# Performance work log

Hardware: AMD Instinct MI355X
Metric: run time of the kernel (lower is better)

The kernel has to match this reference:

```python
import jax, jax.numpy as jnp
import numpy as np


def axisangle2mat(p):
    # p: [N, 6] = (rotation vector rx,ry,rz, translation tx,ty,tz) -> [N, 3, 4]
    v = p[:, :3]
    t = p[:, 3:]
    theta = jnp.sqrt(jnp.sum(v * v, axis=-1) + 1e-12)  # [N]
    k = v / theta[:, None]
    kx, ky, kz = k[:, 0], k[:, 1], k[:, 2]
    zero = jnp.zeros_like(kx)
    K = jnp.stack([
        jnp.stack([zero, -kz, ky], -1),
        jnp.stack([kz, zero, -kx], -1),
        jnp.stack([-ky, kx, zero], -1),
    ], -2)  # [N,3,3]
    I = jnp.eye(3, dtype=p.dtype)
    s = jnp.sin(theta)[:, None, None]
    c = (1.0 - jnp.cos(theta))[:, None, None]
    R = I + s * K + c * jnp.matmul(K, K)
    return jnp.concatenate([R, t[:, :, None]], axis=-1)  # [N,3,4]


def grid_sample_3d(vol, grid):
    # vol: [D,H,W]; grid: [...,3] with last dim (x,y,z) in [-1,1].
    # Replicates F.grid_sample(mode='bilinear', padding_mode='zeros', align_corners=False).
    D, H, W = vol.shape
    ix = ((grid[..., 0] + 1.0) * W - 1.0) * 0.5
    iy = ((grid[..., 1] + 1.0) * H - 1.0) * 0.5
    iz = ((grid[..., 2] + 1.0) * D - 1.0) * 0.5
    x0 = jnp.floor(ix); y0 = jnp.floor(iy); z0 = jnp.floor(iz)
    fx = ix - x0; fy = iy - y0; fz = iz - z0
    vol_flat = vol.reshape(-1)
    out = jnp.zeros(grid.shape[:-1], vol.dtype)
    for dz in (0, 1):
        for dy in (0, 1):
            for dx in (0, 1):
                xc = x0 + dx; yc = y0 + dy; zc = z0 + dz
                wgt = ((fx if dx else 1.0 - fx) * (fy if dy else 1.0 - fy) * (fz if dz else 1.0 - fz))
                valid = ((xc >= 0) & (xc < W) & (yc >= 0) & (yc < H) & (zc >= 0) & (zc < D))
                xi = jnp.clip(xc, 0, W - 1).astype(jnp.int32)
                yi = jnp.clip(yc, 0, H - 1).astype(jnp.int32)
                zi = jnp.clip(zc, 0, D - 1).astype(jnp.int32)
                v = vol_flat[(zi * H + yi) * W + xi]
                out = out + jnp.where(valid, v * wgt, 0.0)
    return out


def setup_inputs() -> dict:
    key = jax.random.key(0)
    ks = jax.random.split(key, 8)
    B, n, D, H, W = 4096, 2048, 256, 256, 256
    x = jax.random.normal(ks[0], (1, 1, D, H, W), dtype=jnp.float32)
    # voxel-space sample points inside the volume
    sampleGrid = jax.random.uniform(ks[1], (B, 3), dtype=jnp.float32) * jnp.array([W - 1, H - 1, D - 1], jnp.float32)
    ax = jnp.concatenate([
        jax.random.normal(ks[2], (B, 1, 3), dtype=jnp.float32) * 0.1,   # small rotations
        jax.random.normal(ks[3], (B, 1, 3), dtype=jnp.float32) * 5.0,   # translations (voxels)
    ], axis=-1)
    low = jax.random.uniform(ks[4], (B, 1, 3), dtype=jnp.float32) * 2.0
    ext = jax.random.uniform(ks[5], (B, 1, 3), dtype=jnp.float32) * 4.0 + 1.0
    bound = jnp.concatenate([low, low + ext], axis=1)  # [B,2,3], bound[:,1] > bound[:,0]
    A = jax.random.normal(ks[6], (B, 3, 3), dtype=jnp.float32) * 0.3
    InvCovScaled = jnp.einsum('bij,bkj->bik', A, A) + 0.5 * jnp.eye(3, dtype=jnp.float32)  # SPD
    xyz_psf = jax.random.normal(ks[7], (B, n, 3), dtype=jnp.float32)
    psf_sigma = jnp.ones((1,), jnp.float32)  # unused in forward (as in the original)
    return dict(x=x, sampleGrid=sampleGrid, ax=ax, bound=bound,
                InvCovScaled=InvCovScaled, psf_sigma=psf_sigma, xyz_psf=xyz_psf)


def reference(x, sampleGrid, ax, bound, InvCovScaled, psf_sigma, xyz_psf):
    # x: [1,1,D,H,W]; sampleGrid: [B,3]; ax: [B,1,6]; bound: [B,2,3];
    # InvCovScaled: [B,3,3]; xyz_psf: [B,n,3] (the torch.randn draw, made explicit)
    W = x.shape[-1]; H = x.shape[-2]; D = x.shape[-3]
    size = (W, H, D)  # matches torch: size = [x.shape[-1], x.shape[-2], x.shape[-3]]
    scaled_xyz_psf = 2.0 * jax.nn.sigmoid(xyz_psf) - 1.0                      # [B,n,3]
    half = (bound[:, 1, :] - bound[:, 0, :]) * 0.5                            # [B,3]
    bound_psf = scaled_xyz_psf * half[:, None]                                # [B,n,3]
    mat = axisangle2mat(ax.reshape(-1, 6)).reshape(ax.shape[:-1] + (3, 4))    # [B,1,3,4]
    R = mat[:, 0, :, :3]                                                      # [B,3,3]
    T = mat[:, 0, :, 3]                                                       # [B,3]
    # trans_first=True: R @ (p + T)
    mat_sampleGrid = jnp.einsum('bij,bj->bi', R, sampleGrid + T)[:, None]     # [B,1,3]
    psf_sampleGrid = mat_sampleGrid + bound_psf                               # [B,n,3]
    norm = jnp.array([size[0] - 1, size[1] - 1, size[2] - 1], psf_sampleGrid.dtype)
    grid = 2.0 * (psf_sampleGrid / norm - 0.5)
    psf_x = grid_sample_3d(x[0, 0], grid)                                     # [B,n]
    # Mahalanobis-style weights: exp(-0.5 * c^T InvCov c)
    q = jnp.einsum('bni,bij,bnj->bn', bound_psf, InvCovScaled, bound_psf)
    w = jnp.exp(-0.5 * q)                                                     # [B,n]
    y = jnp.sum(psf_x * w, axis=-1) / jnp.sum(w, axis=-1)                     # [B]
    return y
```

## Files before the change

kernel.cpp:

```cpp
#include <hip/hip_runtime.h>
#include <math.h>

constexpr int NT   = 256;
constexpr int DIMV = 256;
constexpr int RS   = 8;
constexpr int RROW = 9;
constexpr int RSLICE = RS * RROW;

__global__ __launch_bounds__(NT) void psf_sample_kernel(
    const float* __restrict__ vol,
    const float* __restrict__ sampleGrid,
    const float* __restrict__ ax,
    const float* __restrict__ bound,
    const float* __restrict__ invcov,
    const float* __restrict__ xyz,
    float* __restrict__ out,
    int n)
{
    const int b   = blockIdx.x;
    const int tid = threadIdx.x;

    __shared__ float s_vol[RS * RSLICE];
    __shared__ float s_red[2 * (NT / 64)];

    const float v0 = ax[b*6+0], v1 = ax[b*6+1], v2 = ax[b*6+2];
    const float t0 = ax[b*6+3], t1 = ax[b*6+4], t2 = ax[b*6+5];
    const float theta = sqrtf(v0*v0 + v1*v1 + v2*v2 + 1e-12f);
    const float inv = 1.0f / theta;
    const float kx = v0*inv, ky = v1*inv, kz = v2*inv;
    const float sn = sinf(theta);
    const float cn = 1.0f - cosf(theta);
    const float R00 = 1.0f - cn*(ky*ky + kz*kz);
    const float R01 = -sn*kz + cn*kx*ky;
    const float R02 =  sn*ky + cn*kx*kz;
    const float R10 =  sn*kz + cn*kx*ky;
    const float R11 = 1.0f - cn*(kx*kx + kz*kz);
    const float R12 = -sn*kx + cn*ky*kz;
    const float R20 = -sn*ky + cn*kx*kz;
    const float R21 =  sn*kx + cn*ky*kz;
    const float R22 = 1.0f - cn*(kx*kx + ky*ky);
    const float g0 = sampleGrid[b*3+0] + t0;
    const float g1 = sampleGrid[b*3+1] + t1;
    const float g2 = sampleGrid[b*3+2] + t2;
    const float ms0 = R00*g0 + R01*g1 + R02*g2;
    const float ms1 = R10*g0 + R11*g1 + R12*g2;
    const float ms2 = R20*g0 + R21*g1 + R22*g2;
    const float h0 = (bound[b*6+3] - bound[b*6+0]) * 0.5f;
    const float h1 = (bound[b*6+4] - bound[b*6+1]) * 0.5f;
    const float h2 = (bound[b*6+5] - bound[b*6+2]) * 0.5f;
    const float M00 = invcov[b*9+0], M01 = invcov[b*9+1], M02 = invcov[b*9+2];
    const float M11 = invcov[b*9+4], M12 = invcov[b*9+5], M22 = invcov[b*9+8];

    const float B00 = -0.5f * M00 * h0 * h0;
    const float B11 = -0.5f * M11 * h1 * h1;
    const float B22 = -0.5f * M22 * h2 * h2;
    const float B01 = -M01 * h0 * h1;
    const float B02 = -M02 * h0 * h2;
    const float B12 = -M12 * h1 * h2;

    const float kk = 256.0f / 255.0f;
    const float cix = ms0 * kk - 0.5f;
    const float ciy = ms1 * kk - 0.5f;
    const float ciz = ms2 * kk - 0.5f;
    const float hx = h0 * kk, hy = h1 * kk, hz = h2 * kk;

    const int bx = (int)floorf(cix - hx - 1e-3f);
    const int by = (int)floorf(ciy - hy - 1e-3f);
    const int bz = (int)floorf(ciz - hz - 1e-3f);
    const bool fast = (hx <= 2.9f) && (hy <= 2.9f) && (hz <= 2.9f);

    if (fast) {
        #pragma unroll
        for (int pass = 0; pass < (RS*RS*RS)/NT; ++pass) {
            const int idx = pass * NT + tid;
            const int lx = idx & 7, ly = (idx >> 3) & 7, lz = idx >> 6;
            const int gx = bx + lx, gy = by + ly, gz = bz + lz;
            float v = 0.0f;
            if ((unsigned)gx < (unsigned)DIMV && (unsigned)gy < (unsigned)DIMV &&
                (unsigned)gz < (unsigned)DIMV)
                v = vol[((size_t)gz * DIMV + gy) * DIMV + gx];
            s_vol[(lz * RS + ly) * RROW + lx] = v;
        }
    }
    __syncthreads();

    float sum_wx = 0.0f, sum_w = 0.0f;

    auto doSample = [&](float rx, float ry, float rz) {
        const float ex = __expf(-rx), ey = __expf(-ry), ez = __expf(-rz);
        const float sx = (1.0f - ex) * __builtin_amdgcn_rcpf(1.0f + ex);
        const float sy = (1.0f - ey) * __builtin_amdgcn_rcpf(1.0f + ey);
        const float sz = (1.0f - ez) * __builtin_amdgcn_rcpf(1.0f + ez);

        const float ixf = fmaf(sx, hx, cix);
        const float iyf = fmaf(sy, hy, ciy);
        const float izf = fmaf(sz, hz, ciz);
        const float x0f = floorf(ixf), y0f = floorf(iyf), z0f = floorf(izf);
        const float fx = ixf - x0f, fy = iyf - y0f, fz = izf - z0f;

        float val;
        if (fast) {
            const int lx = (int)x0f - bx;
            const int ly = (int)y0f - by;
            const int lz = (int)z0f - bz;
            const float* p = &s_vol[(lz * RS + ly) * RROW + lx];
            const float v000 = p[0],              v001 = p[1];
            const float v010 = p[RROW],           v011 = p[RROW + 1];
            const float v100 = p[RSLICE],         v101 = p[RSLICE + 1];
            const float v110 = p[RSLICE + RROW],  v111 = p[RSLICE + RROW + 1];
            const float a00 = fmaf(fx, v001 - v000, v000);
            const float a01 = fmaf(fx, v011 - v010, v010);
            const float a10 = fmaf(fx, v101 - v100, v100);
            const float a11 = fmaf(fx, v111 - v110, v110);
            const float a0  = fmaf(fy, a01 - a00, a00);
            const float a1  = fmaf(fy, a11 - a10, a10);
            val = fmaf(fz, a1 - a0, a0);
        } else {
            const int x0 = (int)x0f, y0 = (int)y0f, z0 = (int)z0f;
            const int x1 = x0 + 1, y1 = y0 + 1, z1 = z0 + 1;
            const bool vx0 = (unsigned)x0 < (unsigned)DIMV;
            const bool vx1 = (unsigned)x1 < (unsigned)DIMV;
            const bool vy0 = (unsigned)y0 < (unsigned)DIMV;
            const bool vy1 = (unsigned)y1 < (unsigned)DIMV;
            const bool vz0 = (unsigned)z0 < (unsigned)DIMV;
            const bool vz1 = (unsigned)z1 < (unsigned)DIMV;
            const int cx0 = min(max(x0,0),DIMV-1), cx1 = min(max(x1,0),DIMV-1);
            const int cy0 = min(max(y0,0),DIMV-1), cy1 = min(max(y1,0),DIMV-1);
            const int cz0 = min(max(z0,0),DIMV-1), cz1 = min(max(z1,0),DIMV-1);
            const float wx0 = 1.0f-fx, wx1 = fx, wy0 = 1.0f-fy, wy1 = fy;
            const float wz0 = 1.0f-fz, wz1 = fz;
            const int r00 = (cz0*DIMV + cy0)*DIMV, r01 = (cz0*DIMV + cy1)*DIMV;
            const int r10 = (cz1*DIMV + cy0)*DIMV, r11 = (cz1*DIMV + cy1)*DIMV;
            val  = (vz0&&vy0&&vx0) ? vol[r00+cx0]*(wz0*wy0*wx0) : 0.0f;
            val += (vz0&&vy0&&vx1) ? vol[r00+cx1]*(wz0*wy0*wx1) : 0.0f;
            val += (vz0&&vy1&&vx0) ? vol[r01+cx0]*(wz0*wy1*wx0) : 0.0f;
            val += (vz0&&vy1&&vx1) ? vol[r01+cx1]*(wz0*wy1*wx1) : 0.0f;
            val += (vz1&&vy0&&vx0) ? vol[r10+cx0]*(wz1*wy0*wx0) : 0.0f;
            val += (vz1&&vy0&&vx1) ? vol[r10+cx1]*(wz1*wy0*wx1) : 0.0f;
            val += (vz1&&vy1&&vx0) ? vol[r11+cx0]*(wz1*wy1*wx0) : 0.0f;
            val += (vz1&&vy1&&vx1) ? vol[r11+cx1]*(wz1*wy1*wx1) : 0.0f;
        }

        const float f = fmaf(B00, sx*sx,
                        fmaf(B11, sy*sy,
                        fmaf(B22, sz*sz,
                        fmaf(B01, sx*sy,
                        fmaf(B02, sx*sz, B12 * (sy*sz))))));
        const float w = __expf(f);
        sum_w  += w;
        sum_wx = fmaf(w, val, sum_wx);
    };

    const int ng = n >> 2;
    const float4* __restrict__ xb4 =
        reinterpret_cast<const float4*>(xyz + (size_t)b * n * 3);
    for (int g = tid; g < ng; g += NT) {
        const float4 q0 = xb4[g*3 + 0];
        const float4 q1 = xb4[g*3 + 1];
        const float4 q2 = xb4[g*3 + 2];
        doSample(q0.x, q0.y, q0.z);
        doSample(q0.w, q1.x, q1.y);
        doSample(q1.z, q1.w, q2.x);
        doSample(q2.y, q2.z, q2.w);
    }
    const float* __restrict__ xb = xyz + (size_t)b * n * 3;
    for (int i = (ng << 2) + tid; i < n; i += NT)
        doSample(xb[i*3+0], xb[i*3+1], xb[i*3+2]);

    #pragma unroll
    for (int off = 32; off > 0; off >>= 1) {
        sum_wx += __shfl_down(sum_wx, off);
        sum_w  += __shfl_down(sum_w,  off);
    }
    const int wave = tid >> 6;
    const int lane = tid & 63;
    if (lane == 0) { s_red[wave*2] = sum_wx; s_red[wave*2+1] = sum_w; }
    __syncthreads();
    if (tid == 0) {
        float twx = 0.0f, tw = 0.0f;
        #pragma unroll
        for (int wv = 0; wv < NT/64; ++wv) { twx += s_red[wv*2]; tw += s_red[wv*2+1]; }
        out[b] = twx / tw;
    }
}

extern "C" void kernel_launch(void* const* d_in, const int* in_sizes, int n_in,
                              void* d_out, int out_size, void* d_ws, size_t ws_size,
                              hipStream_t stream) {
    const float* vol        = (const float*)d_in[0];
    const float* sampleGrid = (const float*)d_in[1];
    const float* ax         = (const float*)d_in[2];
    const float* bound      = (const float*)d_in[3];
    const float* invcov     = (const float*)d_in[4];
    const float* xyz        = (const float*)d_in[6];
    float* out              = (float*)d_out;

    const int B = in_sizes[1] / 3;
    const int n = in_sizes[6] / (B * 3);

    psf_sample_kernel<<<B, NT, 0, stream>>>(vol, sampleGrid, ax, bound, invcov,
                                            xyz, out, n);
}
```

Before: 30.02 us.

## Precompute per-batch params in prep kernel and pack trilinear corners as float4 in LDS

Moves the per-batch rotation and covariance setup into a separate prep kernel that writes 16 floats per batch to workspace. The sample kernel reads these, makes them wave-uniform with readfirstlane, and builds a second LDS table of float4 corner quads so each trilinear sample needs two 128-bit LDS reads instead of eight scalar ones. It also folds log2(e) into the quadratic coefficients so exp2 can be used directly, and sets a launch-bounds occupancy hint. This costs an extra kernel launch, an extra LDS pass with a barrier, and more shared memory per block.

```diff
diff --git a/kernel.cpp b/kernel.cpp
--- a/kernel.cpp
+++ b/kernel.cpp
@@ -5,23 +5,30 @@
 constexpr int DIMV = 256;
 constexpr int RS   = 8;
 constexpr int RROW = 9;
-constexpr int RSLICE = RS * RROW;
-
-__global__ __launch_bounds__(NT) void psf_sample_kernel(
-    const float* __restrict__ vol,
+constexpr int SROW = 9;
+constexpr int SSLICE = RS * SROW;
+
+__device__ __forceinline__ float rflf(float x) {
+    return __uint_as_float(__builtin_amdgcn_readfirstlane(__float_as_uint(x)));
+}
+__device__ __forceinline__ float fexp2(float x) {
+#if __has_builtin(__builtin_amdgcn_exp2f)
+    return __builtin_amdgcn_exp2f(x);
+#else
+    return __expf(x * 0.6931471805599453f);
+#endif
+}
+
+__global__ __launch_bounds__(256) void psf_prep_kernel(
     const float* __restrict__ sampleGrid,
     const float* __restrict__ ax,
     const float* __restrict__ bound,
     const float* __restrict__ invcov,
-    const float* __restrict__ xyz,
-    float* __restrict__ out,
-    int n)
+    float* __restrict__ params,
+    int B)
 {
-    const int b   = blockIdx.x;
-    const int tid = threadIdx.x;
-
-    __shared__ float s_vol[RS * RSLICE];
-    __shared__ float s_red[2 * (NT / 64)];
+    const int b = blockIdx.x * blockDim.x + threadIdx.x;
+    if (b >= B) return;
 
     const float v0 = ax[b*6+0], v1 = ax[b*6+1], v2 = ax[b*6+2];
     const float t0 = ax[b*6+3], t1 = ax[b*6+4], t2 = ax[b*6+5];
@@ -51,23 +58,59 @@
     const float M00 = invcov[b*9+0], M01 = invcov[b*9+1], M02 = invcov[b*9+2];
     const float M11 = invcov[b*9+4], M12 = invcov[b*9+5], M22 = invcov[b*9+8];
 
-    const float B00 = -0.5f * M00 * h0 * h0;
-    const float B11 = -0.5f * M11 * h1 * h1;
-    const float B22 = -0.5f * M22 * h2 * h2;
-    const float B01 = -M01 * h0 * h1;
-    const float B02 = -M02 * h0 * h2;
-    const float B12 = -M12 * h1 * h2;
-
+    const float LOG2E = 1.4426950408889634f;
     const float kk = 256.0f / 255.0f;
-    const float cix = ms0 * kk - 0.5f;
-    const float ciy = ms1 * kk - 0.5f;
-    const float ciz = ms2 * kk - 0.5f;
+    const float cix = fmaf(ms0, kk, -0.5f);
+    const float ciy = fmaf(ms1, kk, -0.5f);
+    const float ciz = fmaf(ms2, kk, -0.5f);
     const float hx = h0 * kk, hy = h1 * kk, hz = h2 * kk;
-
     const int bx = (int)floorf(cix - hx - 1e-3f);
     const int by = (int)floorf(ciy - hy - 1e-3f);
     const int bz = (int)floorf(ciz - hz - 1e-3f);
     const bool fast = (hx <= 2.9f) && (hy <= 2.9f) && (hz <= 2.9f);
+
+    float4* p = reinterpret_cast<float4*>(params + (size_t)b * 16);
+    p[0] = make_float4(cix, ciy, ciz, hx);
+    p[1] = make_float4(hy, hz,
+                       -0.5f * M00 * h0 * h0 * LOG2E,
+                       -0.5f * M11 * h1 * h1 * LOG2E);
+    p[2] = make_float4(-0.5f * M22 * h2 * h2 * LOG2E,
+                       -M01 * h0 * h1 * LOG2E,
+                       -M02 * h0 * h2 * LOG2E,
+                       -M12 * h1 * h2 * LOG2E);
+    p[3] = make_float4((float)bx, (float)by, (float)bz, fast ? 1.0f : 0.0f);
+}
+
+__global__ __launch_bounds__(NT, 6) void psf_sample_kernel(
+    const float* __restrict__ vol,
+    const float* __restrict__ params,
+    const float* __restrict__ xyz,
+    float* __restrict__ out,
+    int n)
+{
+    const int b   = blockIdx.x;
+    const int tid = threadIdx.x;
+
+    __shared__ float  s_lin[RS * RS * RROW];
+    __shared__ float4 s_q[(RS*RS - 1) * SROW + RS];
+    __shared__ float  s_red[2 * (NT / 64)];
+
+    const float4* pp = reinterpret_cast<const float4*>(params + (size_t)b * 16);
+    const float4 P0 = pp[0];
+    const float4 P1 = pp[1];
+    const float4 P2 = pp[2];
+    const float4 P3 = pp[3];
+
+    const float cix = rflf(P0.x), ciy = rflf(P0.y), ciz = rflf(P0.z);
+    const float hx  = rflf(P0.w), hy  = rflf(P1.x), hz  = rflf(P1.y);
+    const float Bxx = rflf(P1.z), Byy = rflf(P1.w), Bzz = rflf(P2.x);
+    const float Bxy = rflf(P2.y), Bxz = rflf(P2.z), Byz = rflf(P2.w);
+    const int bx = __builtin_amdgcn_readfirstlane((int)P3.x);
+    const int by = __builtin_amdgcn_readfirstlane((int)P3.y);
+    const int bz = __builtin_amdgcn_readfirstlane((int)P3.z);
+    const bool fast = P3.w > 0.5f;
+    const float addrC = rflf((float)(bz * SSLICE + by * SROW + bx));
+    const float LOG2E = 1.4426950408889634f;
 
     if (fast) {
         #pragma unroll
@@ -79,15 +122,30 @@
             if ((unsigned)gx < (unsigned)DIMV && (unsigned)gy < (unsigned)DIMV &&
                 (unsigned)gz < (unsigned)DIMV)
                 v = vol[((size_t)gz * DIMV + gy) * DIMV + gx];
-            s_vol[(lz * RS + ly) * RROW + lx] = v;
+            s_lin[(lz * RS + ly) * RROW + lx] = v;
         }
+        __syncthreads();
+        #pragma unroll
+        for (int pass = 0; pass < (RS*RS*RS)/NT; ++pass) {
+            const int idx = pass * NT + tid;
+            const int lx = idx & 7, ly = (idx >> 3) & 7, lz = idx >> 6;
+            const int x1 = lx < 7 ? lx + 1 : 7;
+            const int y1 = ly < 7 ? ly + 1 : 7;
+            const int r0 = (lz * RS + ly) * RROW;
+            const int r1 = (lz * RS + y1) * RROW;
+            s_q[(lz * RS + ly) * SROW + lx] =
+                make_float4(s_lin[r0 + lx], s_lin[r0 + x1],
+                            s_lin[r1 + lx], s_lin[r1 + x1]);
+        }
     }
     __syncthreads();
 
     float sum_wx = 0.0f, sum_w = 0.0f;
 
     auto doSample = [&](float rx, float ry, float rz) {
-        const float ex = __expf(-rx), ey = __expf(-ry), ez = __expf(-rz);
+        const float ex = fexp2(rx * -LOG2E);
+        const float ey = fexp2(ry * -LOG2E);
+        const float ez = fexp2(rz * -LOG2E);
         const float sx = (1.0f - ex) * __builtin_amdgcn_rcpf(1.0f + ex);
         const float sy = (1.0f - ey) * __builtin_amdgcn_rcpf(1.0f + ey);
         const float sz = (1.0f - ez) * __builtin_amdgcn_rcpf(1.0f + ez);
@@ -100,19 +158,16 @@
 
         float val;
         if (fast) {
-            const int lx = (int)x0f - bx;
-            const int ly = (int)y0f - by;
-            const int lz = (int)z0f - bz;
-            const float* p = &s_vol[(lz * RS + ly) * RROW + lx];
-            const float v000 = p[0],              v001 = p[1];
-            const float v010 = p[RROW],           v011 = p[RROW + 1];
-            const float v100 = p[RSLICE],         v101 = p[RSLICE + 1];
-            const float v110 = p[RSLICE + RROW],  v111 = p[RSLICE + RROW + 1];
-            const float a00 = fmaf(fx, v001 - v000, v000);
-            const float a01 = fmaf(fx, v011 - v010, v010);
-            const float a10 = fmaf(fx, v101 - v100, v100);
-            const float a11 = fmaf(fx, v111 - v110, v110);
+            const float ef = fmaf(z0f, (float)SSLICE,
+                             fmaf(y0f, (float)SROW, x0f - addrC));
+            const int e = (int)ef;
+            const float4 q0 = s_q[e];
+            const float4 q1 = s_q[e + SSLICE];
+            const float a00 = fmaf(fx, q0.y - q0.x, q0.x);
+            const float a01 = fmaf(fx, q0.w - q0.z, q0.z);
             const float a0  = fmaf(fy, a01 - a00, a00);
+            const float a10 = fmaf(fx, q1.y - q1.x, q1.x);
+            const float a11 = fmaf(fx, q1.w - q1.z, q1.z);
             const float a1  = fmaf(fy, a11 - a10, a10);
             val = fmaf(fz, a1 - a0, a0);
         } else {
@@ -141,12 +196,12 @@
             val += (vz1&&vy1&&vx1) ? vol[r11+cx1]*(wz1*wy1*wx1) : 0.0f;
         }
 
-        const float f = fmaf(B00, sx*sx,
-                        fmaf(B11, sy*sy,
-                        fmaf(B22, sz*sz,
-                        fmaf(B01, sx*sy,
-                        fmaf(B02, sx*sz, B12 * (sy*sz))))));
-        const float w = __expf(f);
+        const float f = fmaf(Bxx, sx*sx,
+                        fmaf(Byy, sy*sy,
+                        fmaf(Bzz, sz*sz,
+                        fmaf(Bxy, sx*sy,
+                        fmaf(Bxz, sx*sz, Byz * (sy*sz))))));
+        const float w = fexp2(f);
         sum_w  += w;
         sum_wx = fmaf(w, val, sum_wx);
     };
@@ -194,10 +249,12 @@
     const float* invcov     = (const float*)d_in[4];
     const float* xyz        = (const float*)d_in[6];
     float* out              = (float*)d_out;
+    float* params           = (float*)d_ws;
 
     const int B = in_sizes[1] / 3;
     const int n = in_sizes[6] / (B * 3);
 
-    psf_sample_kernel<<<B, NT, 0, stream>>>(vol, sampleGrid, ax, bound, invcov,
-                                            xyz, out, n);
-}
+    psf_prep_kernel<<<(B + 255) / 256, 256, 0, stream>>>(sampleGrid, ax, bound,
+                                                         invcov, params, B);
+    psf_sample_kernel<<<B, NT, 0, stream>>>(vol, params, xyz, out, n);
+}
```

New measurement: 33.00 us. 9.9% more time.
